# Kernel tuning notes

Measured on AMD Instinct MI355X. Metric: run time of the kernel, lower is better.

Reference implementation:

```python
import jax, jax.numpy as jnp
import numpy as np

BATCH = 64
DIM_IN = 4096
DIM_OUT = 4096


def setup_inputs() -> dict:
    key = jax.random.key(0)
    kx, km, kt = jax.random.split(key, 3)
    x = jax.random.bernoulli(kx, 0.5, (BATCH, DIM_IN))                      # bool [B, dim_in]
    masks = jax.random.bernoulli(km, 0.5, (DIM_IN, DIM_OUT))                # bool [dim_in, dim_out]
    thresholds = jax.random.randint(kt, (DIM_OUT,), 0, DIM_IN, dtype=jnp.int32)  # int [dim_out]
    return {"x": x, "masks": masks, "thresholds": thresholds}


def reference(x, masks, thresholds):
    # sum_i XNOR(x_i, m_ij) = #(both true) + #(both false)
    #                       = dim_in - sum_i x_i - sum_i m_ij + 2 * (x @ m)
    # This reproduces the broadcast-XNOR + reduce-sum math exactly without
    # materializing the [B, dim_in, dim_out] boolean tensor.
    xi = x.astype(jnp.int32)
    mi = masks.astype(jnp.int32)
    both_true = jnp.einsum('bi,io->bo', xi, mi)                             # int32 [B, dim_out]
    sums = DIM_IN - xi.sum(axis=1, keepdims=True) - mi.sum(axis=0, keepdims=True) + 2 * both_true
    return sums > thresholds[None, :]                                       # bool [B, dim_out]
```

## Files before the change

### kernel.cpp

```cpp
#include <hip/hip_runtime.h>
#include <stdint.h>

#define DIM_IN  4096
#define DIM_OUT 4096
#define BATCH   64

typedef unsigned long long u64;
typedef uint32_t u32;

__device__ __forceinline__ bool is_word_fmt(const u32* __restrict__ p) {
    bool words = true;
#pragma unroll
    for (int i = 0; i < 8; ++i) {
        u32 v = p[i];
        if (v > 1u && v != 0x3F800000u) words = false;
    }
    return words;
}

__global__ __launch_bounds__(256) void pack_kernel(
        const void* __restrict__ masks, const void* __restrict__ x,
        u64* __restrict__ mp, u64* __restrict__ xp) {
    const int bid = blockIdx.x;
    if (bid < 1024) {
        const bool words = is_word_fmt((const u32*)masks);
        const int wid = bid * 4 + (threadIdx.x >> 6);
        const int w   = wid >> 6;
        const int o   = ((wid & 63) << 6) + (threadIdx.x & 63);
        const int row0 = w * 64;

        u64 bits = 0;
        if (words) {
            const u32* pw = (const u32*)masks + (size_t)row0 * DIM_OUT + o;
#pragma unroll
            for (int rb = 0; rb < 4; ++rb) {
                u32 v[16];
#pragma unroll
                for (int r = 0; r < 16; ++r)
                    v[r] = pw[(size_t)(rb * 16 + r) * DIM_OUT];
#pragma unroll
                for (int r = 0; r < 16; ++r)
                    bits |= (u64)(v[r] != 0u) << (rb * 16 + r);
            }
        } else {
            const uint8_t* pb = (const uint8_t*)masks + (size_t)row0 * DIM_OUT + o;
#pragma unroll
            for (int rb = 0; rb < 4; ++rb) {
                uint8_t v[16];
#pragma unroll
                for (int r = 0; r < 16; ++r)
                    v[r] = pb[(size_t)(rb * 16 + r) * DIM_OUT];
#pragma unroll
                for (int r = 0; r < 16; ++r)
                    bits |= (u64)(v[r] != 0u) << (rb * 16 + r);
            }
        }
        mp[(size_t)w * DIM_OUT + o] = bits;
    } else {
        const bool words = is_word_fmt((const u32*)x);
        const int bxid = bid - 1024;
        const int wave = bxid * 4 + (threadIdx.x >> 6);
        const int lane = threadIdx.x & 63;
        const int base = wave * 64;

#pragma unroll 16
        for (int k = 0; k < 64; ++k) {
            const int idx = base + k;
            const size_t e = (size_t)idx * 64 + lane;
            bool pred;
            if (words) pred = ((const u32*)x)[e] != 0u;
            else       pred = ((const uint8_t*)x)[e] != 0u;
            const u64 m = __ballot(pred);
            if (lane == 0) xp[idx] = m;
        }
    }
}

__global__ __launch_bounds__(256) void bnn_kernel(
        const u64* __restrict__ mp, const u64* __restrict__ xp,
        const int* __restrict__ thr, int* __restrict__ out) {
    const int o  = blockIdx.x * 256 + threadIdx.x;
    const int b0 = blockIdx.y * 4;

    const u64* __restrict__ x0 = xp + (size_t)(b0 + 0) * 64;
    const u64* __restrict__ x1 = xp + (size_t)(b0 + 1) * 64;
    const u64* __restrict__ x2 = xp + (size_t)(b0 + 2) * 64;
    const u64* __restrict__ x3 = xp + (size_t)(b0 + 3) * 64;

    int a0 = 0, a1 = 0, a2 = 0, a3 = 0;
#pragma unroll 16
    for (int w = 0; w < 64; ++w) {
        const u64 mw = mp[(size_t)w * DIM_OUT + o];
        a0 += __popcll(x0[w] ^ mw);
        a1 += __popcll(x1[w] ^ mw);
        a2 += __popcll(x2[w] ^ mw);
        a3 += __popcll(x3[w] ^ mw);
    }

    const int t = thr[o];
    out[(size_t)(b0 + 0) * DIM_OUT + o] = (DIM_IN - a0) > t ? 1 : 0;
    out[(size_t)(b0 + 1) * DIM_OUT + o] = (DIM_IN - a1) > t ? 1 : 0;
    out[(size_t)(b0 + 2) * DIM_OUT + o] = (DIM_IN - a2) > t ? 1 : 0;
    out[(size_t)(b0 + 3) * DIM_OUT + o] = (DIM_IN - a3) > t ? 1 : 0;
}

extern "C" void kernel_launch(void* const* d_in, const int* in_sizes, int n_in,
                              void* d_out, int out_size, void* d_ws, size_t ws_size,
                              hipStream_t stream) {
    const void* x     = d_in[0];
    const void* masks = d_in[1];
    const int*  thr   = (const int*)d_in[2];
    int* out = (int*)d_out;

    u64* mp = (u64*)d_ws;
    u64* xp = (u64*)((char*)d_ws + (size_t)64 * DIM_OUT * 8);

    pack_kernel<<<dim3(1040), dim3(256), 0, stream>>>(masks, x, mp, xp);
    bnn_kernel<<<dim3(16, 16), dim3(256), 0, stream>>>(mp, xp, thr, out);
}
```

Measured before the change: 42.41 us.

## Vectorize mask packing with wide row loads and byte-granular packed writes

Restructures the mask-packing stage so each block handles 8 rows of one 64-row word group, and each thread loads 16-byte (or 4-byte for bool) vectors across columns instead of one scalar per row. Each thread accumulates 8 bits per column and writes a single byte of the packed 64-bit word, so eight blocks together fill each word. The goal is fewer, wider, coalesced loads from the large mask array and half as many blocks. The cost is scattered byte stores to the packed buffer, with eight blocks writing different bytes of the same word.

```diff
diff --git a/kernel.cpp b/kernel.cpp
--- a/kernel.cpp
+++ b/kernel.cpp
@@ -22,43 +22,73 @@
         const void* __restrict__ masks, const void* __restrict__ x,
         u64* __restrict__ mp, u64* __restrict__ xp) {
     const int bid = blockIdx.x;
-    if (bid < 1024) {
+    if (bid < 512) {
         const bool words = is_word_fmt((const u32*)masks);
-        const int wid = bid * 4 + (threadIdx.x >> 6);
-        const int w   = wid >> 6;
-        const int o   = ((wid & 63) << 6) + (threadIdx.x & 63);
-        const int row0 = w * 64;
+        const int w = bid >> 3;
+        const int q = bid & 7;
+        const int row0 = w * 64 + q * 8;
+        const int t = threadIdx.x;
 
-        u64 bits = 0;
+        u32 acc[4][4] = {};
+
         if (words) {
-            const u32* pw = (const u32*)masks + (size_t)row0 * DIM_OUT + o;
+            const u32* pw = (const u32*)masks + (size_t)row0 * DIM_OUT + t * 4;
 #pragma unroll
-            for (int rb = 0; rb < 4; ++rb) {
-                u32 v[16];
-#pragma unroll
-                for (int r = 0; r < 16; ++r)
-                    v[r] = pw[(size_t)(rb * 16 + r) * DIM_OUT];
-#pragma unroll
-                for (int r = 0; r < 16; ++r)
-                    bits |= (u64)(v[r] != 0u) << (rb * 16 + r);
+            for (int r = 0; r < 8; ++r) {
+                const size_t ro = (size_t)r * DIM_OUT;
+                const uint4 v0 = *reinterpret_cast<const uint4*>(pw + ro);
+                const uint4 v1 = *reinterpret_cast<const uint4*>(pw + ro + 1024);
+                const uint4 v2 = *reinterpret_cast<const uint4*>(pw + ro + 2048);
+                const uint4 v3 = *reinterpret_cast<const uint4*>(pw + ro + 3072);
+                acc[0][0] |= (u32)(v0.x != 0u) << r;
+                acc[0][1] |= (u32)(v0.y != 0u) << r;
+                acc[0][2] |= (u32)(v0.z != 0u) << r;
+                acc[0][3] |= (u32)(v0.w != 0u) << r;
+                acc[1][0] |= (u32)(v1.x != 0u) << r;
+                acc[1][1] |= (u32)(v1.y != 0u) << r;
+                acc[1][2] |= (u32)(v1.z != 0u) << r;
+                acc[1][3] |= (u32)(v1.w != 0u) << r;
+                acc[2][0] |= (u32)(v2.x != 0u) << r;
+                acc[2][1] |= (u32)(v2.y != 0u) << r;
+                acc[2][2] |= (u32)(v2.z != 0u) << r;
+                acc[2][3] |= (u32)(v2.w != 0u) << r;
+                acc[3][0] |= (u32)(v3.x != 0u) << r;
+                acc[3][1] |= (u32)(v3.y != 0u) << r;
+                acc[3][2] |= (u32)(v3.z != 0u) << r;
+                acc[3][3] |= (u32)(v3.w != 0u) << r;
             }
         } else {
-            const uint8_t* pb = (const uint8_t*)masks + (size_t)row0 * DIM_OUT + o;
+            const u32* pb = (const u32*)((const uint8_t*)masks
+                              + (size_t)row0 * DIM_OUT) + t;
 #pragma unroll
-            for (int rb = 0; rb < 4; ++rb) {
-                uint8_t v[16];
+            for (int r = 0; r < 8; ++r) {
+                const size_t ro = (size_t)r * (DIM_OUT / 4);
+                u32 b[4];
+                b[0] = pb[ro];
+                b[1] = pb[ro + 256];
+                b[2] = pb[ro + 512];
+                b[3] = pb[ro + 768];
 #pragma unroll
-                for (int r = 0; r < 16; ++r)
-                    v[r] = pb[(size_t)(rb * 16 + r) * DIM_OUT];
+                for (int s = 0; s < 4; ++s) {
 #pragma unroll
-                for (int r = 0; r < 16; ++r)
-                    bits |= (u64)(v[r] != 0u) << (rb * 16 + r);
+                    for (int c = 0; c < 4; ++c)
+                        acc[s][c] |= (u32)(((b[s] >> (8 * c)) & 0xFFu) != 0u) << r;
+                }
             }
         }
-        mp[(size_t)w * DIM_OUT + o] = bits;
+
+        uint8_t* mpb = (uint8_t*)mp;
+#pragma unroll
+        for (int s = 0; s < 4; ++s) {
+#pragma unroll
+            for (int c = 0; c < 4; ++c) {
+                const int o = s * 1024 + t * 4 + c;
+                mpb[((size_t)w * DIM_OUT + o) * 8 + q] = (uint8_t)acc[s][c];
+            }
+        }
     } else {
         const bool words = is_word_fmt((const u32*)x);
-        const int bxid = bid - 1024;
+        const int bxid = bid - 512;
         const int wave = bxid * 4 + (threadIdx.x >> 6);
         const int lane = threadIdx.x & 63;
         const int base = wave * 64;
@@ -115,6 +145,6 @@
     u64* mp = (u64*)d_ws;
     u64* xp = (u64*)((char*)d_ws + (size_t)64 * DIM_OUT * 8);
 
-    pack_kernel<<<dim3(1040), dim3(256), 0, stream>>>(masks, x, mp, xp);
+    pack_kernel<<<dim3(528), dim3(256), 0, stream>>>(masks, x, mp, xp);
     bnn_kernel<<<dim3(16, 16), dim3(256), 0, stream>>>(mp, xp, thr, out);
 }
```

Measured after the change: 47.94 us. +13.0%, slower.

## Pack masks as 16-bit chunks with vectorized wide loads per thread

Applied to the files above, without the earlier changes.

The mask packing kernel now has each thread load 4 adjacent output columns with one 16-byte load (or one 4-byte load in byte format) across 16 rows, instead of scalar loads per column. Packed bits are stored as 16-bit pieces in a [256][DIM_OUT] ushort layout, which the popcount kernel reassembles into 64-bit words with four 16-bit loads per step. This is meant to cut the number of memory transactions when reading the large mask input. In exchange the main kernel issues more, narrower loads and the workspace offset for the packed activations moves.

```diff
diff --git a/kernel.cpp b/kernel.cpp
--- a/kernel.cpp
+++ b/kernel.cpp
@@ -20,42 +20,53 @@
 
 __global__ __launch_bounds__(256) void pack_kernel(
         const void* __restrict__ masks, const void* __restrict__ x,
-        u64* __restrict__ mp, u64* __restrict__ xp) {
+        u32* __restrict__ mp16, u64* __restrict__ xp) {
     const int bid = blockIdx.x;
     if (bid < 1024) {
         const bool words = is_word_fmt((const u32*)masks);
-        const int wid = bid * 4 + (threadIdx.x >> 6);
-        const int w   = wid >> 6;
-        const int o   = ((wid & 63) << 6) + (threadIdx.x & 63);
-        const int row0 = w * 64;
+        const int w    = bid >> 4;
+        const int oseg = bid & 15;
+        const int q    = threadIdx.x >> 6;
+        const int lane = threadIdx.x & 63;
+        const int o0   = oseg * 256 + lane * 4;
+        const int row0 = w * 64 + q * 16;
 
-        u64 bits = 0;
+        u32 acc[4] = {0u, 0u, 0u, 0u};
+
         if (words) {
-            const u32* pw = (const u32*)masks + (size_t)row0 * DIM_OUT + o;
+            const u32* base = (const u32*)masks + (size_t)row0 * DIM_OUT + o0;
+            uint4 v[16];
 #pragma unroll
-            for (int rb = 0; rb < 4; ++rb) {
-                u32 v[16];
+            for (int r = 0; r < 16; ++r)
+                v[r] = *reinterpret_cast<const uint4*>(base + (size_t)r * DIM_OUT);
 #pragma unroll
-                for (int r = 0; r < 16; ++r)
-                    v[r] = pw[(size_t)(rb * 16 + r) * DIM_OUT];
-#pragma unroll
-                for (int r = 0; r < 16; ++r)
-                    bits |= (u64)(v[r] != 0u) << (rb * 16 + r);
+            for (int r = 0; r < 16; ++r) {
+                acc[0] |= (u32)(v[r].x != 0u) << r;
+                acc[1] |= (u32)(v[r].y != 0u) << r;
+                acc[2] |= (u32)(v[r].z != 0u) << r;
+                acc[3] |= (u32)(v[r].w != 0u) << r;
             }
         } else {
-            const uint8_t* pb = (const uint8_t*)masks + (size_t)row0 * DIM_OUT + o;
+            const u32* base = (const u32*)((const uint8_t*)masks
+                                + (size_t)row0 * DIM_OUT + o0);
+            u32 v[16];
 #pragma unroll
-            for (int rb = 0; rb < 4; ++rb) {
-                uint8_t v[16];
+            for (int r = 0; r < 16; ++r)
+                v[r] = base[(size_t)r * (DIM_OUT / 4)];
 #pragma unroll
-                for (int r = 0; r < 16; ++r)
-                    v[r] = pb[(size_t)(rb * 16 + r) * DIM_OUT];
-#pragma unroll
-                for (int r = 0; r < 16; ++r)
-                    bits |= (u64)(v[r] != 0u) << (rb * 16 + r);
+            for (int r = 0; r < 16; ++r) {
+                acc[0] |= (u32)((v[r] & 0x000000FFu) != 0u) << r;
+                acc[1] |= (u32)((v[r] & 0x0000FF00u) != 0u) << r;
+                acc[2] |= (u32)((v[r] & 0x00FF0000u) != 0u) << r;
+                acc[3] |= (u32)((v[r] & 0xFF000000u) != 0u) << r;
             }
         }
-        mp[(size_t)w * DIM_OUT + o] = bits;
+
+        const size_t u32idx = (((size_t)(w * 4 + q) * DIM_OUT) + o0) >> 1;
+        uint2 s;
+        s.x = (acc[0] & 0xFFFFu) | (acc[1] << 16);
+        s.y = (acc[2] & 0xFFFFu) | (acc[3] << 16);
+        *reinterpret_cast<uint2*>(mp16 + u32idx) = s;
     } else {
         const bool words = is_word_fmt((const u32*)x);
         const int bxid = bid - 1024;
@@ -77,7 +88,7 @@
 }
 
 __global__ __launch_bounds__(256) void bnn_kernel(
-        const u64* __restrict__ mp, const u64* __restrict__ xp,
+        const ushort* __restrict__ mp16, const u64* __restrict__ xp,
         const int* __restrict__ thr, int* __restrict__ out) {
     const int o  = blockIdx.x * 256 + threadIdx.x;
     const int b0 = blockIdx.y * 4;
@@ -88,9 +99,14 @@
     const u64* __restrict__ x3 = xp + (size_t)(b0 + 3) * 64;
 
     int a0 = 0, a1 = 0, a2 = 0, a3 = 0;
-#pragma unroll 16
+#pragma unroll 8
     for (int w = 0; w < 64; ++w) {
-        const u64 mw = mp[(size_t)w * DIM_OUT + o];
+        const size_t base = (size_t)(w * 4) * DIM_OUT + o;
+        const u64 m0 = mp16[base];
+        const u64 m1 = mp16[base + DIM_OUT];
+        const u64 m2 = mp16[base + 2 * DIM_OUT];
+        const u64 m3 = mp16[base + 3 * DIM_OUT];
+        const u64 mw = m0 | (m1 << 16) | (m2 << 32) | (m3 << 48);
         a0 += __popcll(x0[w] ^ mw);
         a1 += __popcll(x1[w] ^ mw);
         a2 += __popcll(x2[w] ^ mw);
@@ -112,9 +128,9 @@
     const int*  thr   = (const int*)d_in[2];
     int* out = (int*)d_out;
 
-    u64* mp = (u64*)d_ws;
-    u64* xp = (u64*)((char*)d_ws + (size_t)64 * DIM_OUT * 8);
+    u32* mp16 = (u32*)d_ws;
+    u64* xp   = (u64*)((char*)d_ws + (size_t)256 * DIM_OUT * 8);
 
-    pack_kernel<<<dim3(1040), dim3(256), 0, stream>>>(masks, x, mp, xp);
-    bnn_kernel<<<dim3(16, 16), dim3(256), 0, stream>>>(mp, xp, thr, out);
+    pack_kernel<<<dim3(1040), dim3(256), 0, stream>>>(masks, x, mp16, xp);
+    bnn_kernel<<<dim3(16, 16), dim3(256), 0, stream>>>((const ushort*)mp16, xp, thr, out);
 }
```

After: 44.69 us. 5.4% more time.

## Split mask packing into coalesced row-compress and ballot-transpose kernels

Applied to the files above, without the earlier changes.

Mask packing now happens in two steps. A compress kernel reads the mask with wide, fully coalesced uint4 loads and uses ballots to build per-row bit words. A second kernel transposes 64x64 bit tiles with ballots to produce the column-packed layout the popcount kernel expects. This replaces the earlier strided per-column reads and is meant to make the 64MB (word-format) mask read bandwidth-efficient. The cost is an extra launch and a 2MB intermediate round trip.

```diff
diff --git a/kernel.cpp b/kernel.cpp
--- a/kernel.cpp
+++ b/kernel.cpp
@@ -7,6 +7,9 @@
 
 typedef unsigned long long u64;
 typedef uint32_t u32;
+
+#define NBLK1 2048
+#define NTHR  (NBLK1 * 256)
 
 __device__ __forceinline__ bool is_word_fmt(const u32* __restrict__ p) {
     bool words = true;
@@ -18,44 +21,82 @@
     return words;
 }
 
-__global__ __launch_bounds__(256) void pack_kernel(
-        const void* __restrict__ masks, const void* __restrict__ x,
+__global__ __launch_bounds__(256) void compress_kernel(
+        const void* __restrict__ masks, u64* __restrict__ rp) {
+    const bool words = is_word_fmt((const u32*)masks);
+    const int T    = blockIdx.x * 256 + threadIdx.x;
+    const int lane = threadIdx.x & 63;
+
+    if (words) {
+        const uint4* src = (const uint4*)masks;
+        uint4 v[8];
+#pragma unroll
+        for (int it = 0; it < 8; ++it)
+            v[it] = src[(size_t)T + (size_t)it * NTHR];
+#pragma unroll
+        for (int it = 0; it < 8; ++it) {
+            const u64 b0 = __ballot(v[it].x != 0u);
+            const u64 b1 = __ballot(v[it].y != 0u);
+            const u64 b2 = __ballot(v[it].z != 0u);
+            const u64 b3 = __ballot(v[it].w != 0u);
+            const size_t chunk = ((size_t)T + (size_t)it * NTHR) >> 6;
+            if (lane < 4) {
+                const u64 bb = lane == 0 ? b0 : lane == 1 ? b1
+                             : lane == 2 ? b2 : b3;
+                rp[chunk * 4 + lane] = bb;
+            }
+        }
+    } else {
+        const u32* src = (const u32*)masks;
+        u32 v[8];
+#pragma unroll
+        for (int it = 0; it < 8; ++it)
+            v[it] = src[(size_t)T + (size_t)it * NTHR];
+#pragma unroll
+        for (int it = 0; it < 8; ++it) {
+            const u64 b0 = __ballot((v[it] & 0x000000FFu) != 0u);
+            const u64 b1 = __ballot((v[it] & 0x0000FF00u) != 0u);
+            const u64 b2 = __ballot((v[it] & 0x00FF0000u) != 0u);
+            const u64 b3 = __ballot((v[it] & 0xFF000000u) != 0u);
+            const size_t chunk = ((size_t)T + (size_t)it * NTHR) >> 6;
+            if (lane < 4) {
+                const u64 bb = lane == 0 ? b0 : lane == 1 ? b1
+                             : lane == 2 ? b2 : b3;
+                rp[chunk * 4 + lane] = bb;
+            }
+        }
+    }
+}
+
+__global__ __launch_bounds__(256) void transpose_kernel(
+        const u64* __restrict__ rp, const void* __restrict__ x,
         u64* __restrict__ mp, u64* __restrict__ xp) {
     const int bid = blockIdx.x;
     if (bid < 1024) {
-        const bool words = is_word_fmt((const u32*)masks);
-        const int wid = bid * 4 + (threadIdx.x >> 6);
-        const int w   = wid >> 6;
-        const int o   = ((wid & 63) << 6) + (threadIdx.x & 63);
-        const int row0 = w * 64;
+        const int wg   = bid * 4 + (threadIdx.x >> 6);
+        const int w    = wg >> 6;
+        const int oseg = wg & 63;
+        const int r    = threadIdx.x & 63;
+        const int o0   = oseg * 64;
+        const int jbase = (o0 >> 8) * 4;
+        const int Lbase = (o0 & 255) >> 2;
 
-        u64 bits = 0;
-        if (words) {
-            const u32* pw = (const u32*)masks + (size_t)row0 * DIM_OUT + o;
+        const u64* rowp = rp + (size_t)(w * 64 + r) * 64 + jbase;
+        const u64 rw0 = rowp[0];
+        const u64 rw1 = rowp[1];
+        const u64 rw2 = rowp[2];
+        const u64 rw3 = rowp[3];
+
+        u64 mine = 0;
 #pragma unroll
-            for (int rb = 0; rb < 4; ++rb) {
-                u32 v[16];
-#pragma unroll
-                for (int r = 0; r < 16; ++r)
-                    v[r] = pw[(size_t)(rb * 16 + r) * DIM_OUT];
-#pragma unroll
-                for (int r = 0; r < 16; ++r)
-                    bits |= (u64)(v[r] != 0u) << (rb * 16 + r);
-            }
-        } else {
-            const uint8_t* pb = (const uint8_t*)masks + (size_t)row0 * DIM_OUT + o;
-#pragma unroll
-            for (int rb = 0; rb < 4; ++rb) {
-                uint8_t v[16];
-#pragma unroll
-                for (int r = 0; r < 16; ++r)
-                    v[r] = pb[(size_t)(rb * 16 + r) * DIM_OUT];
-#pragma unroll
-                for (int r = 0; r < 16; ++r)
-                    bits |= (u64)(v[r] != 0u) << (rb * 16 + r);
-            }
+        for (int d = 0; d < 64; ++d) {
+            const u64 srcw = (d & 3) == 0 ? rw0 : (d & 3) == 1 ? rw1
+                           : (d & 3) == 2 ? rw2 : rw3;
+            const int sh = Lbase + (d >> 2);
+            const u64 m = __ballot(((srcw >> sh) & 1ull) != 0ull);
+            if (r == d) mine = m;
         }
-        mp[(size_t)w * DIM_OUT + o] = bits;
+        mp[(size_t)w * DIM_OUT + o0 + r] = mine;
     } else {
         const bool words = is_word_fmt((const u32*)x);
         const int bxid = bid - 1024;
@@ -112,9 +153,11 @@
     const int*  thr   = (const int*)d_in[2];
     int* out = (int*)d_out;
 
-    u64* mp = (u64*)d_ws;
-    u64* xp = (u64*)((char*)d_ws + (size_t)64 * DIM_OUT * 8);
+    u64* rp = (u64*)d_ws;
+    u64* mp = (u64*)((char*)d_ws + (size_t)2 * 1024 * 1024);
+    u64* xp = (u64*)((char*)d_ws + (size_t)4 * 1024 * 1024);
 
-    pack_kernel<<<dim3(1040), dim3(256), 0, stream>>>(masks, x, mp, xp);
-    bnn_kernel<<<dim3(16, 16), dim3(256), 0, stream>>>(mp, xp, thr, out);
+    compress_kernel <<<dim3(NBLK1), dim3(256), 0, stream>>>(masks, rp);
+    transpose_kernel<<<dim3(1040),  dim3(256), 0, stream>>>(rp, x, mp, xp);
+    bnn_kernel      <<<dim3(16,16), dim3(256), 0, stream>>>(mp, xp, thr, out);
 }
```

New measurement: 49.58 us. 16.9% more time.
